# Performance work log

Measured on AMD Instinct MI355X. Metric: run time of the kernel, lower is better.

## Reference

```python
import jax, jax.numpy as jnp
import numpy as np
import math

B = 262144
STATE = 6
TOTAL_MEAS = 27
HID = 256
INPUT_DIM = TOTAL_MEAS * 2 + 1 + STATE + 12  # 73
PI = math.pi
NORM_R_SCALE = 500.0 / 150000.0
ANG_IDX = np.array([0, 1, 3, 4, 6, 9, 10, 12, 13, 15, 18, 19, 21, 22, 24])
ANG_MASK = np.zeros((TOTAL_MEAS,), dtype=bool)
ANG_MASK[ANG_IDX] = True


def setup_inputs() -> dict:
    key = jax.random.key(0)
    ks = jax.random.split(key, 16)
    s = lambda fan: 1.0 / math.sqrt(fan)
    inp = {
        "meas": jax.random.normal(ks[0], (B, TOTAL_MEAS), jnp.float32),
        "mask": jnp.ones((B, TOTAL_MEAS), jnp.float32),
        "dt": jax.random.uniform(ks[1], (B,), jnp.float32),
        "baselines": jax.random.normal(ks[2], (B, 12), jnp.float32),
        "x_prev": jax.random.normal(ks[3], (B, STATE), jnp.float32),
        "hx": jnp.zeros((B, HID), jnp.float32),
        # GRU params (torch gate order: r, z, n)
        "W_ih": jax.random.uniform(ks[4], (3 * HID, INPUT_DIM), jnp.float32, -s(HID), s(HID)),
        "W_hh": jax.random.uniform(ks[5], (3 * HID, HID), jnp.float32, -s(HID), s(HID)),
        "b_ih": jax.random.uniform(ks[6], (3 * HID,), jnp.float32, -s(HID), s(HID)),
        "b_hh": jax.random.uniform(ks[7], (3 * HID,), jnp.float32, -s(HID), s(HID)),
        # LayerNorm
        "ln_g": jnp.ones((HID,), jnp.float32),
        "ln_b": jnp.zeros((HID,), jnp.float32),
        # MLP head: 256 -> 256 -> 128 -> 6*27
        "W1": jax.random.uniform(ks[8], (256, HID), jnp.float32, -s(HID), s(HID)),
        "b1": jax.random.uniform(ks[9], (256,), jnp.float32, -s(HID), s(HID)),
        "W2": jax.random.uniform(ks[10], (128, 256), jnp.float32, -s(256), s(256)),
        "b2": jax.random.uniform(ks[11], (128,), jnp.float32, -s(256), s(256)),
        "W3": jax.random.uniform(ks[12], (STATE * TOTAL_MEAS, 128), jnp.float32, -s(128), s(128)),
        "b3": jax.random.uniform(ks[13], (STATE * TOTAL_MEAS,), jnp.float32, -s(128), s(128)),
    }
    return inp


def _wrap_angle(a):
    two_pi = 2.0 * PI
    return a - two_pi * jnp.round(a / two_pi)


def _platform_y_pred(x_rel):
    # x_rel: [B, 6] -> [B, 9] radar/EO measurement
    r_xy = jnp.sqrt(x_rel[:, 0] ** 2 + x_rel[:, 2] ** 2 + 1e-9)
    az = jnp.arctan2(x_rel[:, 2], x_rel[:, 0]) / PI
    el = jnp.arctan2(x_rel[:, 4], r_xy) / PI
    r = jnp.sqrt(x_rel[:, 0] ** 2 + x_rel[:, 2] ** 2 + x_rel[:, 4] ** 2 + 1e-9)
    z = jnp.zeros_like(r)
    return jnp.stack([az, el, r, az, el, z, az, z, z], axis=1)


def _forward(meas, mask, dt, baselines, x_prev, hx,
             W_ih, W_hh, b_ih, b_hh, ln_g, ln_b, W1, b1, W2, b2, W3, b3):
    # f_predict (CV model): x0 += dt*x1, x2 += dt*x3, x4 += dt*x5
    dt_scaled = dt * NORM_R_SCALE  # [B]
    zcol = jnp.zeros_like(x_prev[:, :1])
    shift = jnp.concatenate([x_prev[:, 1:2], zcol, x_prev[:, 3:4], zcol, x_prev[:, 5:6], zcol], axis=1)
    x_minus = x_prev + dt_scaled[:, None] * shift  # [B, 6]

    y_pred = jnp.concatenate([
        _platform_y_pred(x_minus),
        _platform_y_pred(x_minus - baselines[:, 0:6]),
        _platform_y_pred(x_minus - baselines[:, 6:12]),
    ], axis=1)  # [B, 27]

    innov = meas - y_pred
    wrapped = _wrap_angle(innov * PI) / PI
    innov = jnp.where(jnp.asarray(ANG_MASK)[None, :], wrapped, innov)
    innov = innov * mask

    rnn_in = jnp.concatenate([innov, mask, dt[:, None], x_minus, baselines], axis=1)  # [B, 73]

    # single-step GRU (torch semantics, gate order r,z,n)
    gi = rnn_in @ W_ih.T + b_ih  # [B, 3H]
    gh = hx @ W_hh.T + b_hh      # [B, 3H]
    gi_r, gi_z, gi_n = jnp.split(gi, 3, axis=1)
    gh_r, gh_z, gh_n = jnp.split(gh, 3, axis=1)
    r = jax.nn.sigmoid(gi_r + gh_r)
    z = jax.nn.sigmoid(gi_z + gh_z)
    n = jnp.tanh(gi_n + r * gh_n)
    h_new = (1.0 - z) * n + z * hx  # [B, H]

    # LayerNorm
    mu = jnp.mean(h_new, axis=-1, keepdims=True)
    var = jnp.var(h_new, axis=-1, keepdims=True)
    h_ln = (h_new - mu) / jnp.sqrt(var + 1e-5) * ln_g + ln_b

    # MLP gain head (dropout inactive at inference)
    f1 = jax.nn.relu(h_ln @ W1.T + b1)
    f2 = jax.nn.relu(f1 @ W2.T + b2)
    K = (f2 @ W3.T + b3).reshape(-1, STATE, TOTAL_MEAS)
    K = jnp.clip(K, -3.0, 3.0)

    correction = jnp.einsum('bsm,bm->bs', K, innov)
    x_new = jnp.clip(x_minus + correction, -5.0, 5.0)
    return x_new, h_new


def reference(meas, mask, dt, baselines, x_prev, hx,
              W_ih, W_hh, b_ih, b_hh, ln_g, ln_b, W1, b1, W2, b2, W3, b3):
    return _forward(meas, mask, dt, baselines, x_prev, hx,
                    W_ih, W_hh, b_ih, b_hh, ln_g, ln_b, W1, b1, W2, b2, W3, b3)
```

## Files before the change

kernel.cpp:

```cpp
#include <hip/hip_runtime.h>
#include <math.h>

#define B_TOTAL  262144
#define ROWS     64
#define NWG      (B_TOTAL/ROWS)
#define NTHR     256
#define PI_F     3.14159265358979323846f
#define NORM_R   (500.0f/150000.0f)

typedef float  f32x4  __attribute__((ext_vector_type(4)));
typedef short  bf16x8 __attribute__((ext_vector_type(8)));

#define W_TOTAL (49*8192)

#define LDS_RB   0
#define LDS_HB   13312
#define LDS_STG  46080
#define LDS_XMC  78848
#define LDS_TOTAL 80384

#define WAIT_VM4  asm volatile("s_waitcnt vmcnt(4)" ::: "memory")
#define WAIT_VM0  asm volatile("s_waitcnt vmcnt(0)" ::: "memory")
#define WAIT_LGKM asm volatile("s_waitcnt lgkmcnt(0)" ::: "memory")
#define BARv      __builtin_amdgcn_s_barrier()

__device__ __forceinline__ ushort f2bf(float f){
    union { float f; unsigned u; } v; v.f = f;
    unsigned r = v.u + 0x7FFFu + ((v.u >> 16) & 1u);
    return (ushort)(r >> 16);
}
__device__ __forceinline__ float b2f(ushort u){
    union { unsigned u; float f; } v; v.u = ((unsigned)u) << 16;
    return v.f;
}
__device__ __forceinline__ unsigned pk2(float a, float b){
    return (unsigned)f2bf(a) | ((unsigned)f2bf(b) << 16);
}
__device__ __forceinline__ float upk(unsigned u, int hi){
    return b2f((ushort)(hi ? (u >> 16) : (u & 0xffffu)));
}
__device__ __forceinline__ float sigm(float x){ return 1.0f/(1.0f+__expf(-x)); }
__device__ __forceinline__ float tanh_(float x){ return 1.0f - 2.0f/(__expf(2.0f*x)+1.0f); }
__device__ __forceinline__ int swzb(int row, int k){
    return ((row<<9) + (k<<1)) ^ ((row&7)<<4);
}
__device__ __forceinline__ bf16x8 rdW(const char* gb, int col, int lk){
    int slot = lk ^ ((col >> 1) & 3);
    return *(const bf16x8*)(gb + col*64 + slot*16);
}
__device__ __forceinline__ void stage16(const ushort* src, char* dst, int w, int lane){
    #pragma unroll
    for (int i = 0; i < 4; ++i)
        __builtin_amdgcn_global_load_lds(
            (const __attribute__((address_space(1))) void*)(src + (size_t)((w*4+i)*64 + lane)*8),
            (__attribute__((address_space(3))) void*)(dst + (w*4+i)*1024),
            16, 0, 0);
}
#define PH(g) do { \
    if ((g) < 48) stage16(ws + (size_t)((g)+1)*8192, STG + (((g)+1)&1)*16384, w, lane); \
    if ((g) < 48) WAIT_VM4; else WAIT_VM0; \
    BARv; \
} while(0)

__device__ __forceinline__ void ldA4_rb(const ushort* Rbu, int lr, int kb, int lk8, bf16x8 a[4]){
    #pragma unroll
    for (int i = 0; i < 4; ++i)
        a[i] = *(const bf16x8*)(Rbu + (i*16 + lr)*104 + kb*32 + lk8);
}
__device__ __forceinline__ void ldA4_hb(const char* Hb, int lr, int kb, int lk8, bf16x8 a[4]){
    #pragma unroll
    for (int i = 0; i < 4; ++i)
        a[i] = *(const bf16x8*)(Hb + swzb(i*16 + lr, kb*32 + lk8));
}
__device__ __forceinline__ void mmW(const char* base, int colbase, int lr, int lk,
                                    const bf16x8 a[4], f32x4 acc[4][4]){
    #pragma unroll
    for (int j = 0; j < 4; ++j) {
        bf16x8 wf = rdW(base, colbase + j*16 + lr, lk);
        #pragma unroll
        for (int i = 0; i < 4; ++i)
            acc[i][j] = __builtin_amdgcn_mfma_f32_16x16x32_bf16(wf, a[i], acc[i][j], 0,0,0);
    }
}

__global__ void prep_weights(const float* __restrict__ W_ih, const float* __restrict__ W_hh,
                             const float* __restrict__ W1, const float* __restrict__ W2,
                             const float* __restrict__ W3, ushort* __restrict__ ws)
{
    int id = blockIdx.x*256 + threadIdx.x;
    if (id >= W_TOTAL) return;
    int g = id >> 13;
    int u = id & 8191;
    float v = 0.0f;
    if (g >= 41 && g < 45) {
        int half = u >> 12, u2 = u & 4095;
        int col = u2 >> 5, v5 = u2 & 31, slot = v5 >> 3, e = v5 & 7;
        int kq = slot ^ ((col >> 1) & 3);
        int kb = (g-41)*2 + half;
        v = W2[col*256 + kb*32 + kq*8 + e];
    } else {
        int col = u >> 5, v5 = u & 31, slot = v5 >> 3, e = v5 & 7;
        int kq = slot ^ ((col >> 1) & 3);
        if (g < 3) {
            int k = g*32 + kq*8 + e;
            if (k < 73) v = W_ih[(512+col)*73 + k];
        } else if (g < 11) {
            int k = (g-3)*32 + kq*8 + e;
            v = W_hh[(512+col)*256 + k];
        } else if (g < 22) {
            int k = (g-11)*32 + kq*8 + e;
            v = (k < 73) ? W_ih[col*73 + k] : ((k < 96) ? 0.0f : W_hh[col*256 + (k-96)]);
        } else if (g < 33) {
            int k = (g-22)*32 + kq*8 + e;
            v = (k < 73) ? W_ih[(256+col)*73 + k] : ((k < 96) ? 0.0f : W_hh[(256+col)*256 + (k-96)]);
        } else if (g < 41) {
            int k = (g-33)*32 + kq*8 + e;
            v = W1[col*256 + k];
        } else {
            int k = (g-45)*32 + kq*8 + e;
            if (col < 162) v = W3[col*128 + k];
        }
    }
    ws[id] = f2bf(v);
}

__global__ __launch_bounds__(NTHR, 2) void knet_mfma(
    const float* __restrict__ meas, const float* __restrict__ mask,
    const float* __restrict__ dt,   const float* __restrict__ baselines,
    const float* __restrict__ x_prev, const float* __restrict__ hx,
    const float* __restrict__ b_ih, const float* __restrict__ b_hh,
    const float* __restrict__ ln_g, const float* __restrict__ ln_b,
    const float* __restrict__ b1,   const float* __restrict__ b2,
    const float* __restrict__ b3,
    const ushort* __restrict__ ws,
    float* __restrict__ out)
{
    extern __shared__ char smem[];
    ushort* Rbu  = (ushort*)(smem + LDS_RB);
    char*   Hb   = smem + LDS_HB;
    char*   STG  = smem + LDS_STG;
    float*  xmc  = (float*)(smem + LDS_XMC);

    const int tid  = threadIdx.x;
    const int w    = __builtin_amdgcn_readfirstlane(tid >> 6);
    const int nq   = w;
    const int lane = tid & 63;
    const int lr   = lane & 15;
    const int lk   = lane >> 4;
    const int lk8  = lk * 8;
    const int row0 = blockIdx.x * ROWS;
    float* hout = out + (size_t)B_TOTAL*6;

    stage16(ws, STG, w, lane);

    float* scr = (float*)Hb;
    {
        const size_t m0 = (size_t)row0*27;
        for (int i = tid; i < 1728; i += NTHR) scr[i]        = meas[m0 + i];
        for (int i = tid; i < 1728; i += NTHR) scr[1728 + i] = mask[m0 + i];
        for (int i = tid; i < 768;  i += NTHR) scr[3456 + i] = baselines[(size_t)row0*12 + i];
        for (int i = tid; i < 384;  i += NTHR) scr[4224 + i] = x_prev[(size_t)row0*6 + i];
        if (tid < 64) scr[4608 + tid] = dt[row0 + tid];
    }
    __syncthreads();

    {
        const int row = lane;
        const float dtv = scr[4608 + row];
        const float dts = dtv * NORM_R;
        float xp[6], xm[6];
        #pragma unroll
        for (int s = 0; s < 6; ++s) xp[s] = scr[4224 + row*6 + s];
        xm[0] = xp[0] + dts*xp[1]; xm[1] = xp[1];
        xm[2] = xp[2] + dts*xp[3]; xm[3] = xp[3];
        xm[4] = xp[4] + dts*xp[5]; xm[5] = xp[5];
        if (w < 3) {
            float xr[6];
            #pragma unroll
            for (int s = 0; s < 6; ++s) {
                float b = (w == 0) ? 0.0f : scr[3456 + row*12 + (w-1)*6 + s];
                xr[s] = xm[s] - b;
            }
            float rxy = sqrtf(xr[0]*xr[0] + xr[2]*xr[2] + 1e-9f);
            float azv = atan2f(xr[2], xr[0]) * (1.0f/PI_F);
            float elv = atan2f(xr[4], rxy)   * (1.0f/PI_F);
            float rrv = sqrtf(xr[0]*xr[0] + xr[2]*xr[2] + xr[4]*xr[4] + 1e-9f);
            float y[9] = {azv, elv, rrv, azv, elv, 0.0f, azv, 0.0f, 0.0f};
            const bool ang[9] = {true,true,false,true,true,false,true,false,false};
            #pragma unroll
            for (int i = 0; i < 9; ++i) {
                int m = w*9 + i;
                float ms = scr[1728 + row*27 + m];
                float v  = scr[row*27 + m] - y[i];
                if (ang[i]) v = v - 2.0f*rintf(v*0.5f);
                v *= ms;
                Rbu[row*104 + m]      = f2bf(v);
                Rbu[row*104 + 27 + m] = f2bf(ms);
            }
        } else {
            Rbu[row*104 + 54] = f2bf(dtv);
            #pragma unroll
            for (int s = 0; s < 6; ++s) Rbu[row*104 + 55 + s] = f2bf(xm[s]);
            #pragma unroll
            for (int q = 0; q < 12; ++q) Rbu[row*104 + 61 + q] = f2bf(scr[3456 + row*12 + q]);
            #pragma unroll
            for (int k = 73; k < 96; ++k) Rbu[row*104 + k] = 0;
            #pragma unroll
            for (int s = 0; s < 6; ++s) xmc[row*6 + s] = xm[s];
        }
    }
    __syncthreads();

    {
        const size_t hbase = (size_t)row0 * 256;
        #pragma unroll
        for (int ii = 0; ii < 8; ++ii) {
            int cid = tid + ii*NTHR;
            int r  = cid >> 5;
            int k0 = (cid & 31) << 3;
            const float4* p = (const float4*)(hx + hbase + (size_t)r*256 + k0);
            float4 u = p[0], v2 = p[1];
            bf16x8 o;
            o[0]=(short)f2bf(u.x);  o[1]=(short)f2bf(u.y);  o[2]=(short)f2bf(u.z);  o[3]=(short)f2bf(u.w);
            o[4]=(short)f2bf(v2.x); o[5]=(short)f2bf(v2.y); o[6]=(short)f2bf(v2.z); o[7]=(short)f2bf(v2.w);
            *(bf16x8*)(Hb + swzb(r, k0)) = o;
        }
    }
    __syncthreads();

    unsigned ginp[4][2], ghnp[4][2], npk[4][2];
    unsigned ginq[4][4][2], ghnq[4][4][2];

    {
        f32x4 acc[4][4];
        #pragma unroll
        for (int i = 0; i < 4; ++i)
            #pragma unroll
            for (int j = 0; j < 4; ++j) acc[i][j] = (f32x4){0,0,0,0};
        #pragma unroll
        for (int p = 0; p < 3; ++p) {
            PH(p);
            bf16x8 a[4];
            ldA4_rb(Rbu, lr, p, lk8, a);
            __builtin_amdgcn_s_setprio(1);
            mmW(STG + (p&1)*16384, nq*64, lr, lk, a, acc);
            __builtin_amdgcn_s_setprio(0);
            BARv;
        }
        #pragma unroll
        for (int j = 0; j < 4; ++j) {
            const int c0 = nq*64 + j*16 + lk*4;
            f32x4 b4 = *(const f32x4*)(b_ih + 512 + c0);
            #pragma unroll
            for (int i = 0; i < 4; ++i) {
                ginq[i][j][0] = pk2(acc[i][j][0] + b4[0], acc[i][j][1] + b4[1]);
                ginq[i][j][1] = pk2(acc[i][j][2] + b4[2], acc[i][j][3] + b4[3]);
            }
        }
    }
    {
        f32x4 acc[4][4];
        #pragma unroll
        for (int i = 0; i < 4; ++i)
            #pragma unroll
            for (int j = 0; j < 4; ++j) acc[i][j] = (f32x4){0,0,0,0};
        #pragma unroll
        for (int p = 0; p < 8; ++p) {
            PH(3+p);
            bf16x8 a[4];
            ldA4_hb(Hb, lr, p, lk8, a);
            __builtin_amdgcn_s_setprio(1);
            mmW(STG + ((3+p)&1)*16384, nq*64, lr, lk, a, acc);
            __builtin_amdgcn_s_setprio(0);
            BARv;
        }
        #pragma unroll
        for (int j = 0; j < 4; ++j) {
            const int c0 = nq*64 + j*16 + lk*4;
            f32x4 b4 = *(const f32x4*)(b_hh + 512 + c0);
            #pragma unroll
            for (int i = 0; i < 4; ++i) {
                ghnq[i][j][0] = pk2(acc[i][j][0] + b4[0], acc[i][j][1] + b4[1]);
                ghnq[i][j][1] = pk2(acc[i][j][2] + b4[2], acc[i][j][3] + b4[3]);
            }
        }
    }
    unsigned nq_[4][4][2];
    {
        f32x4 acc[4][4];
        #pragma unroll
        for (int i = 0; i < 4; ++i)
            #pragma unroll
            for (int j = 0; j < 4; ++j) acc[i][j] = (f32x4){0,0,0,0};
        #pragma unroll
        for (int p = 0; p < 11; ++p) {
            PH(11+p);
            bf16x8 a[4];
            if (p < 3) ldA4_rb(Rbu, lr, p, lk8, a);
            else       ldA4_hb(Hb, lr, p-3, lk8, a);
            __builtin_amdgcn_s_setprio(1);
            mmW(STG + ((11+p)&1)*16384, nq*64, lr, lk, a, acc);
            __builtin_amdgcn_s_setprio(0);
            BARv;
        }
        #pragma unroll
        for (int j = 0; j < 4; ++j) {
            const int c0 = nq*64 + j*16 + lk*4;
            f32x4 bi4 = *(const f32x4*)(b_ih + c0);
            f32x4 bh4 = *(const f32x4*)(b_hh + c0);
            #pragma unroll
            for (int i = 0; i < 4; ++i) {
                float nv[4];
                #pragma unroll
                for (int e = 0; e < 4; ++e) {
                    float rg = sigm(acc[i][j][e] + bi4[e] + bh4[e]);
                    nv[e] = tanh_(upk(ginq[i][j][e>>1], e&1) + rg*upk(ghnq[i][j][e>>1], e&1));
                }
                nq_[i][j][0] = pk2(nv[0], nv[1]);
                nq_[i][j][1] = pk2(nv[2], nv[3]);
            }
        }
    }
    {
        f32x4 acc[4][4];
        #pragma unroll
        for (int i = 0; i < 4; ++i)
            #pragma unroll
            for (int j = 0; j < 4; ++j) acc[i][j] = (f32x4){0,0,0,0};
        #pragma unroll
        for (int p = 0; p < 11; ++p) {
            PH(22+p);
            bf16x8 a[4];
            if (p < 3) ldA4_rb(Rbu, lr, p, lk8, a);
            else       ldA4_hb(Hb, lr, p-3, lk8, a);
            __builtin_amdgcn_s_setprio(1);
            mmW(STG + ((22+p)&1)*16384, nq*64, lr, lk, a, acc);
            __builtin_amdgcn_s_setprio(0);
            BARv;
        }
        #pragma unroll
        for (int j = 0; j < 4; ++j) {
            const int c0 = nq*64 + j*16 + lk*4;
            f32x4 bi4 = *(const f32x4*)(b_ih + 256 + c0);
            f32x4 bh4 = *(const f32x4*)(b_hh + 256 + c0);
            #pragma unroll
            for (int i = 0; i < 4; ++i) {
                const int row = i*16 + lr;
                uint2 hxd = *(const uint2*)(Hb + swzb(row, c0));
                float hn4[4];
                #pragma unroll
                for (int e = 0; e < 4; ++e) {
                    float zg = sigm(acc[i][j][e] + bi4[e] + bh4[e]);
                    float hxv = upk(e < 2 ? hxd.x : hxd.y, e&1);
                    hn4[e] = (1.0f - zg)*upk(nq_[i][j][e>>1], e&1) + zg*hxv;
                }
                uint2 o; o.x = pk2(hn4[0], hn4[1]); o.y = pk2(hn4[2], hn4[3]);
                *(uint2*)(Hb + swzb(row, c0)) = o;
                float4 st = { hn4[0], hn4[1], hn4[2], hn4[3] };
                *(float4*)(hout + (size_t)(row0+row)*256 + c0) = st;
            }
        }
    }
    WAIT_LGKM; BARv;

    {
        const int row = tid >> 2;
        const int o   = tid & 3;
        bf16x8 ch[8];
        float sum = 0.0f, sq = 0.0f;
        #pragma unroll
        for (int jx = 0; jx < 8; ++jx) {
            ch[jx] = *(const bf16x8*)(Hb + swzb(row, o*64 + jx*8));
            #pragma unroll
            for (int e = 0; e < 8; ++e) {
                float f = b2f((ushort)ch[jx][e]);
                sum += f; sq += f*f;
            }
        }
        sum += __shfl_xor(sum, 1); sum += __shfl_xor(sum, 2);
        sq  += __shfl_xor(sq, 1);  sq  += __shfl_xor(sq, 2);
        float mu   = sum * (1.0f/256.0f);
        float rstd = rsqrtf(sq*(1.0f/256.0f) - mu*mu + 1e-5f);
        #pragma unroll
        for (int jx = 0; jx < 8; ++jx) {
            int col0 = o*64 + jx*8;
            float4 g0 = *(const float4*)(ln_g + col0), g1 = *(const float4*)(ln_g + col0 + 4);
            float4 bb0 = *(const float4*)(ln_b + col0), bb1 = *(const float4*)(ln_b + col0 + 4);
            bf16x8 oo;
            oo[0] = (short)f2bf((b2f((ushort)ch[jx][0]) - mu)*rstd*g0.x + bb0.x);
            oo[1] = (short)f2bf((b2f((ushort)ch[jx][1]) - mu)*rstd*g0.y + bb0.y);
            oo[2] = (short)f2bf((b2f((ushort)ch[jx][2]) - mu)*rstd*g0.z + bb0.z);
            oo[3] = (short)f2bf((b2f((ushort)ch[jx][3]) - mu)*rstd*g0.w + bb0.w);
            oo[4] = (short)f2bf((b2f((ushort)ch[jx][4]) - mu)*rstd*g1.x + bb1.x);
            oo[5] = (short)f2bf((b2f((ushort)ch[jx][5]) - mu)*rstd*g1.y + bb1.y);
            oo[6] = (short)f2bf((b2f((ushort)ch[jx][6]) - mu)*rstd*g1.z + bb1.z);
            oo[7] = (short)f2bf((b2f((ushort)ch[jx][7]) - mu)*rstd*g1.w + bb1.w);
            *(bf16x8*)(Hb + swzb(row, col0)) = oo;
        }
    }
    WAIT_LGKM; BARv;

    {
        f32x4 acc[4][4];
        #pragma unroll
        for (int i = 0; i < 4; ++i)
            #pragma unroll
            for (int j = 0; j < 4; ++j) acc[i][j] = (f32x4){0,0,0,0};
        #pragma unroll
        for (int p = 0; p < 8; ++p) {
            PH(33+p);
            bf16x8 a[4];
            ldA4_hb(Hb, lr, p, lk8, a);
            __builtin_amdgcn_s_setprio(1);
            mmW(STG + ((33+p)&1)*16384, nq*64, lr, lk, a, acc);
            __builtin_amdgcn_s_setprio(0);
            BARv;
        }
        #pragma unroll
        for (int j = 0; j < 4; ++j) {
            const int c0 = nq*64 + j*16 + lk*4;
            f32x4 b4 = *(const f32x4*)(b1 + c0);
            #pragma unroll
            for (int i = 0; i < 4; ++i) {
                const int row = i*16 + lr;
                uint2 o;
                o.x = pk2(fmaxf(acc[i][j][0]+b4[0],0.f), fmaxf(acc[i][j][1]+b4[1],0.f));
                o.y = pk2(fmaxf(acc[i][j][2]+b4[2],0.f), fmaxf(acc[i][j][3]+b4[3],0.f));
                *(uint2*)(Hb + swzb(row, c0)) = o;
            }
        }
    }
    WAIT_LGKM; BARv;

    f32x4 c3[4][2];
    #pragma unroll
    for (int i = 0; i < 4; ++i)
        #pragma unroll
        for (int j = 0; j < 2; ++j) c3[i][j] = (f32x4){0,0,0,0};
    #pragma unroll
    for (int p = 0; p < 4; ++p) {
        PH(41+p);
        const char* sb = STG + ((41+p)&1)*16384;
        #pragma unroll
        for (int h = 0; h < 2; ++h) {
            bf16x8 a[4];
            ldA4_hb(Hb, lr, 2*p + h, lk8, a);
            __builtin_amdgcn_s_setprio(1);
            #pragma unroll
            for (int j = 0; j < 2; ++j) {
                bf16x8 wf = rdW(sb + h*8192, nq*32 + j*16 + lr, lk);
                #pragma unroll
                for (int i = 0; i < 4; ++i)
                    c3[i][j] = __builtin_amdgcn_mfma_f32_16x16x32_bf16(wf, a[i], c3[i][j], 0,0,0);
            }
            __builtin_amdgcn_s_setprio(0);
        }
        BARv;
    }
    ushort* F2 = (ushort*)Hb;
    #pragma unroll
    for (int j = 0; j < 2; ++j) {
        const int c0 = nq*32 + j*16 + lk*4;
        f32x4 b4 = *(const f32x4*)(b2 + c0);
        #pragma unroll
        for (int i = 0; i < 4; ++i) {
            const int row = i*16 + lr;
            uint2 o;
            o.x = pk2(fmaxf(c3[i][j][0]+b4[0],0.f), fmaxf(c3[i][j][1]+b4[1],0.f));
            o.y = pk2(fmaxf(c3[i][j][2]+b4[2],0.f), fmaxf(c3[i][j][3]+b4[3],0.f));
            *(uint2*)((char*)F2 + row*272 + c0*2) = o;
        }
    }
    WAIT_LGKM; BARv;

    {
        f32x4 c4[4][3];
        #pragma unroll
        for (int i = 0; i < 4; ++i)
            #pragma unroll
            for (int j = 0; j < 3; ++j) c4[i][j] = (f32x4){0,0,0,0};
        #pragma unroll
        for (int p = 0; p < 4; ++p) {
            PH(45+p);
            const char* sb = STG + ((45+p)&1)*16384;
            bf16x8 a[4];
            #pragma unroll
            for (int i = 0; i < 4; ++i)
                a[i] = *(const bf16x8*)((const char*)F2 + (i*16 + lr)*272 + (p*32 + lk8)*2);
            __builtin_amdgcn_s_setprio(1);
            #pragma unroll
            for (int j = 0; j < 3; ++j) {
                bf16x8 wf = rdW(sb, nq*48 + j*16 + lr, lk);
                #pragma unroll
                for (int i = 0; i < 4; ++i)
                    c4[i][j] = __builtin_amdgcn_mfma_f32_16x16x32_bf16(wf, a[i], c4[i][j], 0,0,0);
            }
            __builtin_amdgcn_s_setprio(0);
            BARv;
        }
        #pragma unroll
        for (int j = 0; j < 3; ++j)
            #pragma unroll
            for (int i = 0; i < 4; ++i) {
                const int row = i*16 + lr;
                #pragma unroll
                for (int e = 0; e < 4; ++e) {
                    int col = nq*48 + j*16 + lk*4 + e;
                    if (col < 162) {
                        int s = col / 27, m = col - s*27;
                        float K = fminf(fmaxf(c4[i][j][e] + b3[col], -3.0f), 3.0f);
                        atomicAdd(&xmc[row*6 + s], K * b2f(Rbu[row*104 + m]));
                    }
                }
            }
    }
    __syncthreads();

    for (int t = tid; t < ROWS*6; t += NTHR) {
        int row = t / 6, s = t - row*6;
        float v = fminf(fmaxf(xmc[t], -5.0f), 5.0f);
        out[(size_t)(row0+row)*6 + s] = v;
    }
}

extern "C" void kernel_launch(void* const* d_in, const int* in_sizes, int n_in,
                              void* d_out, int out_size, void* d_ws, size_t ws_size,
                              hipStream_t stream) {
    const float* meas      = (const float*)d_in[0];
    const float* mask      = (const float*)d_in[1];
    const float* dtv       = (const float*)d_in[2];
    const float* baselines = (const float*)d_in[3];
    const float* x_prev    = (const float*)d_in[4];
    const float* hx        = (const float*)d_in[5];
    const float* W_ih      = (const float*)d_in[6];
    const float* W_hh      = (const float*)d_in[7];
    const float* b_ih      = (const float*)d_in[8];
    const float* b_hh      = (const float*)d_in[9];
    const float* ln_g      = (const float*)d_in[10];
    const float* ln_b      = (const float*)d_in[11];
    const float* W1        = (const float*)d_in[12];
    const float* b1        = (const float*)d_in[13];
    const float* W2        = (const float*)d_in[14];
    const float* b2        = (const float*)d_in[15];
    const float* W3        = (const float*)d_in[16];
    const float* b3        = (const float*)d_in[17];
    ushort* wsb = (ushort*)d_ws;
    float* outp = (float*)d_out;

    prep_weights<<<(W_TOTAL + 255)/256, 256, 0, stream>>>(W_ih, W_hh, W1, W2, W3, wsb);
    knet_mfma<<<NWG, NTHR, LDS_TOTAL, stream>>>(
        meas, mask, dtv, baselines, x_prev, hx,
        b_ih, b_hh, ln_g, ln_b, b1, b2, b3, wsb, outp);
}
```

Baseline: 701.8 us.

## Double workgroup to 512 threads, halve per-wave MFMA tiles, simplify staging sync

Raises the block from 4 to 8 waves so that each wave owns 32 output columns instead of 64. This halves the accumulator and packed-gate register footprint, and launch bounds move to 4 blocks per CU to raise occupancy. The weight staging pipeline changes from a vmcnt(4) partial wait after issuing the next prefetch to a full vmcnt(0) wait plus barrier before issuing it. That shrinks the overlap of global-to-LDS copies with MFMA work and adds more barriers across more waves. LDS use per block is unchanged, so the higher occupancy may be capped by LDS capacity.

```diff
diff --git a/kernel.cpp b/kernel.cpp
--- a/kernel.cpp
+++ b/kernel.cpp
@@ -4,7 +4,7 @@
 #define B_TOTAL  262144
 #define ROWS     64
 #define NWG      (B_TOTAL/ROWS)
-#define NTHR     256
+#define NTHR     512
 #define PI_F     3.14159265358979323846f
 #define NORM_R   (500.0f/150000.0f)
 
@@ -19,9 +19,7 @@
 #define LDS_XMC  78848
 #define LDS_TOTAL 80384
 
-#define WAIT_VM4  asm volatile("s_waitcnt vmcnt(4)" ::: "memory")
 #define WAIT_VM0  asm volatile("s_waitcnt vmcnt(0)" ::: "memory")
-#define WAIT_LGKM asm volatile("s_waitcnt lgkmcnt(0)" ::: "memory")
 #define BARv      __builtin_amdgcn_s_barrier()
 
 __device__ __forceinline__ ushort f2bf(float f){
@@ -44,22 +42,21 @@
 __device__ __forceinline__ int swzb(int row, int k){
     return ((row<<9) + (k<<1)) ^ ((row&7)<<4);
 }
-__device__ __forceinline__ bf16x8 rdW(const char* gb, int col, int lk){
+__device__ __forceinline__ bf16x8 rdW(const char* base, int col, int lk){
     int slot = lk ^ ((col >> 1) & 3);
-    return *(const bf16x8*)(gb + col*64 + slot*16);
+    return *(const bf16x8*)(base + col*64 + slot*16);
 }
 __device__ __forceinline__ void stage16(const ushort* src, char* dst, int w, int lane){
     #pragma unroll
-    for (int i = 0; i < 4; ++i)
+    for (int i = 0; i < 2; ++i)
         __builtin_amdgcn_global_load_lds(
-            (const __attribute__((address_space(1))) void*)(src + (size_t)((w*4+i)*64 + lane)*8),
-            (__attribute__((address_space(3))) void*)(dst + (w*4+i)*1024),
+            (const __attribute__((address_space(1))) void*)(src + (size_t)((w*2+i)*64 + lane)*8),
+            (__attribute__((address_space(3))) void*)(dst + (w*2+i)*1024),
             16, 0, 0);
 }
 #define PH(g) do { \
+    WAIT_VM0; BARv; \
     if ((g) < 48) stage16(ws + (size_t)((g)+1)*8192, STG + (((g)+1)&1)*16384, w, lane); \
-    if ((g) < 48) WAIT_VM4; else WAIT_VM0; \
-    BARv; \
 } while(0)
 
 __device__ __forceinline__ void ldA4_rb(const ushort* Rbu, int lr, int kb, int lk8, bf16x8 a[4]){
@@ -71,16 +68,6 @@
     #pragma unroll
     for (int i = 0; i < 4; ++i)
         a[i] = *(const bf16x8*)(Hb + swzb(i*16 + lr, kb*32 + lk8));
-}
-__device__ __forceinline__ void mmW(const char* base, int colbase, int lr, int lk,
-                                    const bf16x8 a[4], f32x4 acc[4][4]){
-    #pragma unroll
-    for (int j = 0; j < 4; ++j) {
-        bf16x8 wf = rdW(base, colbase + j*16 + lr, lk);
-        #pragma unroll
-        for (int i = 0; i < 4; ++i)
-            acc[i][j] = __builtin_amdgcn_mfma_f32_16x16x32_bf16(wf, a[i], acc[i][j], 0,0,0);
-    }
 }
 
 __global__ void prep_weights(const float* __restrict__ W_ih, const float* __restrict__ W_hh,
@@ -124,7 +111,7 @@
     ws[id] = f2bf(v);
 }
 
-__global__ __launch_bounds__(NTHR, 2) void knet_mfma(
+__global__ __launch_bounds__(NTHR, 4) void knet_mfma(
     const float* __restrict__ meas, const float* __restrict__ mask,
     const float* __restrict__ dt,   const float* __restrict__ baselines,
     const float* __restrict__ x_prev, const float* __restrict__ hx,
@@ -143,11 +130,11 @@
 
     const int tid  = threadIdx.x;
     const int w    = __builtin_amdgcn_readfirstlane(tid >> 6);
-    const int nq   = w;
     const int lane = tid & 63;
     const int lr   = lane & 15;
     const int lk   = lane >> 4;
     const int lk8  = lk * 8;
+    const int cw   = w * 32;
     const int row0 = blockIdx.x * ROWS;
     float* hout = out + (size_t)B_TOTAL*6;
 
@@ -164,7 +151,7 @@
     }
     __syncthreads();
 
-    {
+    if (w < 4) {
         const int row = lane;
         const float dtv = scr[4608 + row];
         const float dts = dtv * NORM_R;
@@ -214,7 +201,7 @@
     {
         const size_t hbase = (size_t)row0 * 256;
         #pragma unroll
-        for (int ii = 0; ii < 8; ++ii) {
+        for (int ii = 0; ii < 4; ++ii) {
             int cid = tid + ii*NTHR;
             int r  = cid >> 5;
             int k0 = (cid & 31) << 3;
@@ -228,84 +215,100 @@
     }
     __syncthreads();
 
-    unsigned ginp[4][2], ghnp[4][2], npk[4][2];
-    unsigned ginq[4][4][2], ghnq[4][4][2];
-
-    {
-        f32x4 acc[4][4];
+    unsigned gipk[4][2][2], ghpk[4][2][2], npk[4][2][2];
+
+    {
+        f32x4 acc[4][2];
         #pragma unroll
         for (int i = 0; i < 4; ++i)
             #pragma unroll
-            for (int j = 0; j < 4; ++j) acc[i][j] = (f32x4){0,0,0,0};
+            for (int j = 0; j < 2; ++j) acc[i][j] = (f32x4){0,0,0,0};
         #pragma unroll
         for (int p = 0; p < 3; ++p) {
             PH(p);
+            const char* sb = STG + ((p&1)<<14);
             bf16x8 a[4];
             ldA4_rb(Rbu, lr, p, lk8, a);
             __builtin_amdgcn_s_setprio(1);
-            mmW(STG + (p&1)*16384, nq*64, lr, lk, a, acc);
+            #pragma unroll
+            for (int j = 0; j < 2; ++j) {
+                bf16x8 b = rdW(sb, cw + j*16 + lr, lk);
+                #pragma unroll
+                for (int i = 0; i < 4; ++i)
+                    acc[i][j] = __builtin_amdgcn_mfma_f32_16x16x32_bf16(b, a[i], acc[i][j], 0,0,0);
+            }
             __builtin_amdgcn_s_setprio(0);
-            BARv;
-        }
-        #pragma unroll
-        for (int j = 0; j < 4; ++j) {
-            const int c0 = nq*64 + j*16 + lk*4;
+        }
+        #pragma unroll
+        for (int j = 0; j < 2; ++j) {
+            const int c0 = cw + j*16 + lk*4;
             f32x4 b4 = *(const f32x4*)(b_ih + 512 + c0);
             #pragma unroll
             for (int i = 0; i < 4; ++i) {
-                ginq[i][j][0] = pk2(acc[i][j][0] + b4[0], acc[i][j][1] + b4[1]);
-                ginq[i][j][1] = pk2(acc[i][j][2] + b4[2], acc[i][j][3] + b4[3]);
-            }
-        }
-    }
-    {
-        f32x4 acc[4][4];
+                gipk[i][j][0] = pk2(acc[i][j][0] + b4[0], acc[i][j][1] + b4[1]);
+                gipk[i][j][1] = pk2(acc[i][j][2] + b4[2], acc[i][j][3] + b4[3]);
+            }
+        }
+    }
+    {
+        f32x4 acc[4][2];
         #pragma unroll
         for (int i = 0; i < 4; ++i)
             #pragma unroll
-            for (int j = 0; j < 4; ++j) acc[i][j] = (f32x4){0,0,0,0};
+            for (int j = 0; j < 2; ++j) acc[i][j] = (f32x4){0,0,0,0};
         #pragma unroll
         for (int p = 0; p < 8; ++p) {
             PH(3+p);
+            const char* sb = STG + (((3+p)&1)<<14);
             bf16x8 a[4];
             ldA4_hb(Hb, lr, p, lk8, a);
             __builtin_amdgcn_s_setprio(1);
-            mmW(STG + ((3+p)&1)*16384, nq*64, lr, lk, a, acc);
+            #pragma unroll
+            for (int j = 0; j < 2; ++j) {
+                bf16x8 b = rdW(sb, cw + j*16 + lr, lk);
+                #pragma unroll
+                for (int i = 0; i < 4; ++i)
+                    acc[i][j] = __builtin_amdgcn_mfma_f32_16x16x32_bf16(b, a[i], acc[i][j], 0,0,0);
+            }
             __builtin_amdgcn_s_setprio(0);
-            BARv;
-        }
-        #pragma unroll
-        for (int j = 0; j < 4; ++j) {
-            const int c0 = nq*64 + j*16 + lk*4;
+        }
+        #pragma unroll
+        for (int j = 0; j < 2; ++j) {
+            const int c0 = cw + j*16 + lk*4;
             f32x4 b4 = *(const f32x4*)(b_hh + 512 + c0);
             #pragma unroll
             for (int i = 0; i < 4; ++i) {
-                ghnq[i][j][0] = pk2(acc[i][j][0] + b4[0], acc[i][j][1] + b4[1]);
-                ghnq[i][j][1] = pk2(acc[i][j][2] + b4[2], acc[i][j][3] + b4[3]);
-            }
-        }
-    }
-    unsigned nq_[4][4][2];
-    {
-        f32x4 acc[4][4];
+                ghpk[i][j][0] = pk2(acc[i][j][0] + b4[0], acc[i][j][1] + b4[1]);
+                ghpk[i][j][1] = pk2(acc[i][j][2] + b4[2], acc[i][j][3] + b4[3]);
+            }
+        }
+    }
+    {
+        f32x4 acc[4][2];
         #pragma unroll
         for (int i = 0; i < 4; ++i)
             #pragma unroll
-            for (int j = 0; j < 4; ++j) acc[i][j] = (f32x4){0,0,0,0};
+            for (int j = 0; j < 2; ++j) acc[i][j] = (f32x4){0,0,0,0};
         #pragma unroll
         for (int p = 0; p < 11; ++p) {
             PH(11+p);
+            const char* sb = STG + (((11+p)&1)<<14);
             bf16x8 a[4];
             if (p < 3) ldA4_rb(Rbu, lr, p, lk8, a);
             else       ldA4_hb(Hb, lr, p-3, lk8, a);
             __builtin_amdgcn_s_setprio(1);
-            mmW(STG + ((11+p)&1)*16384, nq*64, lr, lk, a, acc);
+            #pragma unroll
+            for (int j = 0; j < 2; ++j) {
+                bf16x8 b = rdW(sb, cw + j*16 + lr, lk);
+                #pragma unroll
+                for (int i = 0; i < 4; ++i)
+                    acc[i][j] = __builtin_amdgcn_mfma_f32_16x16x32_bf16(b, a[i], acc[i][j], 0,0,0);
+            }
             __builtin_amdgcn_s_setprio(0);
-            BARv;
-        }
-        #pragma unroll
-        for (int j = 0; j < 4; ++j) {
-            const int c0 = nq*64 + j*16 + lk*4;
+        }
+        #pragma unroll
+        for (int j = 0; j < 2; ++j) {
+            const int c0 = cw + j*16 + lk*4;
             f32x4 bi4 = *(const f32x4*)(b_ih + c0);
             f32x4 bh4 = *(const f32x4*)(b_hh + c0);
             #pragma unroll
@@ -314,76 +317,82 @@
                 #pragma unroll
                 for (int e = 0; e < 4; ++e) {
                     float rg = sigm(acc[i][j][e] + bi4[e] + bh4[e]);
-                    nv[e] = tanh_(upk(ginq[i][j][e>>1], e&1) + rg*upk(ghnq[i][j][e>>1], e&1));
+                    nv[e] = tanh_(upk(gipk[i][j][e>>1], e&1) + rg*upk(ghpk[i][j][e>>1], e&1));
                 }
-                nq_[i][j][0] = pk2(nv[0], nv[1]);
-                nq_[i][j][1] = pk2(nv[2], nv[3]);
-            }
-        }
-    }
-    {
-        f32x4 acc[4][4];
-        #pragma unroll
-        for (int i = 0; i < 4; ++i)
-            #pragma unroll
-            for (int j = 0; j < 4; ++j) acc[i][j] = (f32x4){0,0,0,0};
-        #pragma unroll
-        for (int p = 0; p < 11; ++p) {
-            PH(22+p);
-            bf16x8 a[4];
-            if (p < 3) ldA4_rb(Rbu, lr, p, lk8, a);
-            else       ldA4_hb(Hb, lr, p-3, lk8, a);
-            __builtin_amdgcn_s_setprio(1);
-            mmW(STG + ((22+p)&1)*16384, nq*64, lr, lk, a, acc);
-            __builtin_amdgcn_s_setprio(0);
-            BARv;
-        }
-        #pragma unroll
-        for (int j = 0; j < 4; ++j) {
-            const int c0 = nq*64 + j*16 + lk*4;
-            f32x4 bi4 = *(const f32x4*)(b_ih + 256 + c0);
-            f32x4 bh4 = *(const f32x4*)(b_hh + 256 + c0);
-            #pragma unroll
-            for (int i = 0; i < 4; ++i) {
-                const int row = i*16 + lr;
-                uint2 hxd = *(const uint2*)(Hb + swzb(row, c0));
-                float hn4[4];
-                #pragma unroll
-                for (int e = 0; e < 4; ++e) {
-                    float zg = sigm(acc[i][j][e] + bi4[e] + bh4[e]);
-                    float hxv = upk(e < 2 ? hxd.x : hxd.y, e&1);
-                    hn4[e] = (1.0f - zg)*upk(nq_[i][j][e>>1], e&1) + zg*hxv;
-                }
-                uint2 o; o.x = pk2(hn4[0], hn4[1]); o.y = pk2(hn4[2], hn4[3]);
-                *(uint2*)(Hb + swzb(row, c0)) = o;
-                float4 st = { hn4[0], hn4[1], hn4[2], hn4[3] };
-                *(float4*)(hout + (size_t)(row0+row)*256 + c0) = st;
-            }
-        }
-    }
-    WAIT_LGKM; BARv;
-
-    {
-        const int row = tid >> 2;
-        const int o   = tid & 3;
-        bf16x8 ch[8];
+                npk[i][j][0] = pk2(nv[0], nv[1]);
+                npk[i][j][1] = pk2(nv[2], nv[3]);
+            }
+        }
+    }
+    f32x4 zacc[4][2];
+    #pragma unroll
+    for (int i = 0; i < 4; ++i)
+        #pragma unroll
+        for (int j = 0; j < 2; ++j) zacc[i][j] = (f32x4){0,0,0,0};
+    #pragma unroll
+    for (int p = 0; p < 11; ++p) {
+        PH(22+p);
+        const char* sb = STG + (((22+p)&1)<<14);
+        bf16x8 a[4];
+        if (p < 3) ldA4_rb(Rbu, lr, p, lk8, a);
+        else       ldA4_hb(Hb, lr, p-3, lk8, a);
+        __builtin_amdgcn_s_setprio(1);
+        #pragma unroll
+        for (int j = 0; j < 2; ++j) {
+            bf16x8 b = rdW(sb, cw + j*16 + lr, lk);
+            #pragma unroll
+            for (int i = 0; i < 4; ++i)
+                zacc[i][j] = __builtin_amdgcn_mfma_f32_16x16x32_bf16(b, a[i], zacc[i][j], 0,0,0);
+        }
+        __builtin_amdgcn_s_setprio(0);
+    }
+    __syncthreads();
+
+    #pragma unroll
+    for (int j = 0; j < 2; ++j) {
+        const int c0 = cw + j*16 + lk*4;
+        f32x4 biz = *(const f32x4*)(b_ih + 256 + c0);
+        f32x4 bhz = *(const f32x4*)(b_hh + 256 + c0);
+        #pragma unroll
+        for (int i = 0; i < 4; ++i) {
+            const int row = i*16 + lr;
+            uint2 hxd = *(const uint2*)(Hb + swzb(row, c0));
+            float hn4[4];
+            #pragma unroll
+            for (int e = 0; e < 4; ++e) {
+                float zg = sigm(zacc[i][j][e] + biz[e] + bhz[e]);
+                float hxv = upk(e < 2 ? hxd.x : hxd.y, e&1);
+                hn4[e] = (1.0f - zg)*upk(npk[i][j][e>>1], e&1) + zg*hxv;
+            }
+            uint2 o; o.x = pk2(hn4[0], hn4[1]); o.y = pk2(hn4[2], hn4[3]);
+            *(uint2*)(Hb + swzb(row, c0)) = o;
+            float4 st = { hn4[0], hn4[1], hn4[2], hn4[3] };
+            *(float4*)(hout + (size_t)(row0+row)*256 + c0) = st;
+        }
+    }
+    __syncthreads();
+
+    {
+        const int row = tid >> 3;
+        const int o   = tid & 7;
+        bf16x8 ch[4];
         float sum = 0.0f, sq = 0.0f;
         #pragma unroll
-        for (int jx = 0; jx < 8; ++jx) {
-            ch[jx] = *(const bf16x8*)(Hb + swzb(row, o*64 + jx*8));
+        for (int jx = 0; jx < 4; ++jx) {
+            ch[jx] = *(const bf16x8*)(Hb + swzb(row, o*32 + jx*8));
             #pragma unroll
             for (int e = 0; e < 8; ++e) {
                 float f = b2f((ushort)ch[jx][e]);
                 sum += f; sq += f*f;
             }
         }
-        sum += __shfl_xor(sum, 1); sum += __shfl_xor(sum, 2);
-        sq  += __shfl_xor(sq, 1);  sq  += __shfl_xor(sq, 2);
+        sum += __shfl_xor(sum, 1); sum += __shfl_xor(sum, 2); sum += __shfl_xor(sum, 4);
+        sq  += __shfl_xor(sq, 1);  sq  += __shfl_xor(sq, 2);  sq  += __shfl_xor(sq, 4);
         float mu   = sum * (1.0f/256.0f);
         float rstd = rsqrtf(sq*(1.0f/256.0f) - mu*mu + 1e-5f);
         #pragma unroll
-        for (int jx = 0; jx < 8; ++jx) {
-            int col0 = o*64 + jx*8;
+        for (int jx = 0; jx < 4; ++jx) {
+            int col0 = o*32 + jx*8;
             float4 g0 = *(const float4*)(ln_g + col0), g1 = *(const float4*)(ln_g + col0 + 4);
             float4 bb0 = *(const float4*)(ln_b + col0), bb1 = *(const float4*)(ln_b + col0 + 4);
             bf16x8 oo;
@@ -398,27 +407,34 @@
             *(bf16x8*)(Hb + swzb(row, col0)) = oo;
         }
     }
-    WAIT_LGKM; BARv;
-
-    {
-        f32x4 acc[4][4];
+    __syncthreads();
+
+    {
+        f32x4 acc[4][2];
         #pragma unroll
         for (int i = 0; i < 4; ++i)
             #pragma unroll
-            for (int j = 0; j < 4; ++j) acc[i][j] = (f32x4){0,0,0,0};
+            for (int j = 0; j < 2; ++j) acc[i][j] = (f32x4){0,0,0,0};
         #pragma unroll
         for (int p = 0; p < 8; ++p) {
             PH(33+p);
+            const char* sb = STG + (((33+p)&1)<<14);
             bf16x8 a[4];
             ldA4_hb(Hb, lr, p, lk8, a);
             __builtin_amdgcn_s_setprio(1);
-            mmW(STG + ((33+p)&1)*16384, nq*64, lr, lk, a, acc);
+            #pragma unroll
+            for (int j = 0; j < 2; ++j) {
+                bf16x8 b = rdW(sb, cw + j*16 + lr, lk);
+                #pragma unroll
+                for (int i = 0; i < 4; ++i)
+                    acc[i][j] = __builtin_amdgcn_mfma_f32_16x16x32_bf16(b, a[i], acc[i][j], 0,0,0);
+            }
             __builtin_amdgcn_s_setprio(0);
-            BARv;
-        }
-        #pragma unroll
-        for (int j = 0; j < 4; ++j) {
-            const int c0 = nq*64 + j*16 + lk*4;
+        }
+        __syncthreads();
+        #pragma unroll
+        for (int j = 0; j < 2; ++j) {
+            const int c0 = cw + j*16 + lk*4;
             f32x4 b4 = *(const f32x4*)(b1 + c0);
             #pragma unroll
             for (int i = 0; i < 4; ++i) {
@@ -430,82 +446,75 @@
             }
         }
     }
-    WAIT_LGKM; BARv;
-
-    f32x4 c3[4][2];
-    #pragma unroll
-    for (int i = 0; i < 4; ++i)
-        #pragma unroll
-        for (int j = 0; j < 2; ++j) c3[i][j] = (f32x4){0,0,0,0};
+    __syncthreads();
+
+    f32x4 c3[4];
+    #pragma unroll
+    for (int i = 0; i < 4; ++i) c3[i] = (f32x4){0,0,0,0};
     #pragma unroll
     for (int p = 0; p < 4; ++p) {
         PH(41+p);
-        const char* sb = STG + ((41+p)&1)*16384;
+        const char* sb = STG + (((41+p)&1)<<14);
         #pragma unroll
         for (int h = 0; h < 2; ++h) {
             bf16x8 a[4];
             ldA4_hb(Hb, lr, 2*p + h, lk8, a);
+            bf16x8 b = rdW(sb + h*8192, w*16 + lr, lk);
             __builtin_amdgcn_s_setprio(1);
             #pragma unroll
-            for (int j = 0; j < 2; ++j) {
-                bf16x8 wf = rdW(sb + h*8192, nq*32 + j*16 + lr, lk);
-                #pragma unroll
-                for (int i = 0; i < 4; ++i)
-                    c3[i][j] = __builtin_amdgcn_mfma_f32_16x16x32_bf16(wf, a[i], c3[i][j], 0,0,0);
-            }
+            for (int i = 0; i < 4; ++i)
+                c3[i] = __builtin_amdgcn_mfma_f32_16x16x32_bf16(b, a[i], c3[i], 0,0,0);
             __builtin_amdgcn_s_setprio(0);
         }
-        BARv;
-    }
+    }
+    __syncthreads();
     ushort* F2 = (ushort*)Hb;
-    #pragma unroll
-    for (int j = 0; j < 2; ++j) {
-        const int c0 = nq*32 + j*16 + lk*4;
+    {
+        const int c0 = w*16 + lk*4;
         f32x4 b4 = *(const f32x4*)(b2 + c0);
         #pragma unroll
         for (int i = 0; i < 4; ++i) {
             const int row = i*16 + lr;
             uint2 o;
-            o.x = pk2(fmaxf(c3[i][j][0]+b4[0],0.f), fmaxf(c3[i][j][1]+b4[1],0.f));
-            o.y = pk2(fmaxf(c3[i][j][2]+b4[2],0.f), fmaxf(c3[i][j][3]+b4[3],0.f));
+            o.x = pk2(fmaxf(c3[i][0]+b4[0],0.f), fmaxf(c3[i][1]+b4[1],0.f));
+            o.y = pk2(fmaxf(c3[i][2]+b4[2],0.f), fmaxf(c3[i][3]+b4[3],0.f));
             *(uint2*)((char*)F2 + row*272 + c0*2) = o;
         }
     }
-    WAIT_LGKM; BARv;
-
-    {
-        f32x4 c4[4][3];
+    __syncthreads();
+
+    {
+        f32x4 c4[4][2];
         #pragma unroll
         for (int i = 0; i < 4; ++i)
             #pragma unroll
-            for (int j = 0; j < 3; ++j) c4[i][j] = (f32x4){0,0,0,0};
+            for (int j = 0; j < 2; ++j) c4[i][j] = (f32x4){0,0,0,0};
         #pragma unroll
         for (int p = 0; p < 4; ++p) {
             PH(45+p);
-            const char* sb = STG + ((45+p)&1)*16384;
+            const char* sb = STG + (((45+p)&1)<<14);
             bf16x8 a[4];
             #pragma unroll
             for (int i = 0; i < 4; ++i)
                 a[i] = *(const bf16x8*)((const char*)F2 + (i*16 + lr)*272 + (p*32 + lk8)*2);
             __builtin_amdgcn_s_setprio(1);
             #pragma unroll
-            for (int j = 0; j < 3; ++j) {
-                bf16x8 wf = rdW(sb, nq*48 + j*16 + lr, lk);
+            for (int j = 0; j < 2; ++j) {
+                bf16x8 b = rdW(sb, cw + j*16 + lr, lk);
                 #pragma unroll
                 for (int i = 0; i < 4; ++i)
-                    c4[i][j] = __builtin_amdgcn_mfma_f32_16x16x32_bf16(wf, a[i], c4[i][j], 0,0,0);
+                    c4[i][j] = __builtin_amdgcn_mfma_f32_16x16x32_bf16(b, a[i], c4[i][j], 0,0,0);
             }
             __builtin_amdgcn_s_setprio(0);
-            BARv;
-        }
-        #pragma unroll
-        for (int j = 0; j < 3; ++j)
+        }
+        #pragma unroll
+        for (int j = 0; j < 2; ++j)
             #pragma unroll
             for (int i = 0; i < 4; ++i) {
                 const int row = i*16 + lr;
                 #pragma unroll
                 for (int e = 0; e < 4; ++e) {
-                    int col = nq*48 + j*16 + lk*4 + e;
+                    int col = cw + j*16 + lk*4 + e;
                     if (col < 162) {
                         int s = col / 27, m = col - s*27;
                         float K = fminf(fmaxf(c4[i][j][e] + b3[col], -3.0f), 3.0f);
```

Result: slower. 804.4 us (+14.6%).
